# Kernel tuning notes

Hardware: AMD Instinct MI355X
Metric: run time of the kernel (lower is better)

The kernel has to match this reference:

```python
import jax, jax.numpy as jnp
import numpy as np
from jax import lax

OC, IC, K = 256, 256, 3
PAD, STRIDE = 1, 1
NNZ = 59000
N, H, W = 32, 56, 56


def setup_inputs() -> dict:
    key = jax.random.key(0)
    k1, k2, k3, k4 = jax.random.split(key, 4)
    x = jax.random.normal(k1, (N, IC, H, W), dtype=jnp.float32)
    W_val = jax.random.normal(k2, (NNZ,), dtype=jnp.float32)
    W_idx = jax.random.randint(k3, (NNZ,), 0, OC * IC * K * K, dtype=jnp.int64)
    bias = jax.random.normal(k4, (OC,), dtype=jnp.float32)
    return {"x": x, "W_val": W_val, "W_idx": W_idx, "bias": bias}


def reference(x, W_val, W_idx, bias):
    # Scatter COO values into the dense [OC, IC, K, K] weight (duplicates sum).
    dense_w = jnp.zeros((OC * IC * K * K,), dtype=W_val.dtype).at[W_idx].add(W_val)
    dense_w = dense_w.reshape(OC, IC, K, K)
    # conv2d, NCHW / OIHW layout, stride=STRIDE, symmetric padding=PAD
    out = lax.conv_general_dilated(
        x, dense_w,
        window_strides=(STRIDE, STRIDE),
        padding=[(PAD, PAD), (PAD, PAD)],
        dimension_numbers=("NCHW", "OIHW", "NCHW"),
    )
    out = out + bias[None, :, None, None]
    return out
```

## Files before the change

### kernel.cpp

```cpp
#include <hip/hip_runtime.h>

typedef unsigned short ushort;
typedef __attribute__((ext_vector_type(8))) short bf16x8;
typedef __attribute__((ext_vector_type(4))) float f32x4;
typedef __attribute__((ext_vector_type(4))) ushort us4;

#define NBATCH 32
#define ICN 256
#define OCN 256
#define HSZ 56
#define WSZ 56
#define HP 58
#define SPAT (HP*HP)
#define KTOT 2304
#define MTOT (NBATCH*HSZ*WSZ)
#define NT   (KTOT/64)
#define BM   224

#define XP_BYTES ((size_t)NBATCH*SPAT*ICN*2)
#define WD_BYTES ((size_t)OCN*KTOT*4)

__device__ __forceinline__ ushort f2bf(float f) {
  union { float f; unsigned u; } c; c.f = f;
  unsigned r = c.u + 0x7FFFu + ((c.u >> 16) & 1u);
  return (ushort)(r >> 16);
}

__global__ void k_transpose(const float* __restrict__ x, ushort* __restrict__ xp) {
  __shared__ ushort t2[WSZ*264];
  int h = blockIdx.x, n = blockIdx.y;
  ushort* dst = xp + ((size_t)n*SPAT + (size_t)h*HP)*ICN;
  if (h == 0 || h == HP-1) {
    for (int e = threadIdx.x; e < HP*ICN/4; e += 256) ((us4*)dst)[e] = (us4){0,0,0,0};
    return;
  }
  const float* src = x + ((size_t)n*ICN*HSZ*WSZ) + (size_t)(h-1)*WSZ;
  for (int e = threadIdx.x; e < ICN*WSZ; e += 256) {
    int ic = e / WSZ, w = e - ic*WSZ;
    t2[w*264 + ic] = f2bf(src[(size_t)ic*(HSZ*WSZ) + w]);
  }
  __syncthreads();
  for (int e4 = threadIdx.x; e4 < HP*ICN/4; e4 += 256) {
    int wp = e4 >> 6, ic4 = (e4 & 63) << 2;
    us4 v = (wp == 0 || wp == HP-1) ? (us4){0,0,0,0}
                                    : *(const us4*)&t2[(wp-1)*264 + ic4];
    ((us4*)dst)[e4] = v;
  }
}

__global__ void k_scatter(const int* __restrict__ idx, const float* __restrict__ val,
                          float* __restrict__ wd, int nnz) {
  int i = blockIdx.x*256 + threadIdx.x;
  if (i >= nnz) return;
  int id = idx[i];
  int oc = id / (ICN*9);
  int rem = id - oc*(ICN*9);
  int ic = rem / 9;
  int k9 = rem - ic*9;
  atomicAdd(wd + (size_t)oc*KTOT + k9*ICN + ic, val[i]);
}

__global__ void k_convert3(const float* __restrict__ wd, ushort* __restrict__ bm3) {
  int e = blockIdx.x*256 + threadIdx.x;
  int lam = e & 63;
  int f   = (e >> 6) & 3;
  int wc  = (e >> 8) & 3;
  int kh  = (e >> 10) & 1;
  int t   = e >> 11;
  int oc  = wc*64 + f*16 + (lam & 15);
  int k   = (t >> 2)*256 + (t & 3)*64 + kh*32 + (lam >> 4)*8;
  const float* src = wd + (size_t)oc*KTOT + k;
  float4 v0 = *(const float4*)(src);
  float4 v1 = *(const float4*)(src + 4);
  us4 lo, hi;
  lo[0]=f2bf(v0.x); lo[1]=f2bf(v0.y); lo[2]=f2bf(v0.z); lo[3]=f2bf(v0.w);
  hi[0]=f2bf(v1.x); hi[1]=f2bf(v1.y); hi[2]=f2bf(v1.z); hi[3]=f2bf(v1.w);
  ushort* dst = bm3 + (size_t)e*8;
  *(us4*)(dst) = lo; *(us4*)(dst+4) = hi;
}


#define GLD(gsrc, ldst) __builtin_amdgcn_global_load_lds( \
    (const __attribute__((address_space(1))) void*)(gsrc), \
    (__attribute__((address_space(3))) void*)(ldst), 16, 0, 0)
#define BAR()  asm volatile("s_barrier" ::: "memory")
#define VMW(N) do { asm volatile("s_waitcnt vmcnt(" #N ")" ::: "memory"); \
                    __builtin_amdgcn_sched_barrier(0); } while (0)
#define LGKM(N) do { asm volatile("s_waitcnt lgkmcnt(" #N ")" ::: "memory"); \
                     __builtin_amdgcn_sched_barrier(0); } while (0)

#define BUF_US  14848
#define BUF_B   29696

#define STAGE2X(T2, PAIR, BUFUS) do { \
    const int t4_ = (T2) >> 2; const int khh_ = t4_/3, khw_ = t4_ - khh_*3; \
    const int koff_ = (khh_*HP + khw_)*256 + (((T2) & 3) << 6); \
    ushort* b_ = Ab + (BUFUS); \
    GLD(xp + ((PAIR) ? sA2 : sA0) + koff_, b_ + ((PAIR) ? dO2 : dO0)); \
    GLD(xp + ((PAIR) ? sA3 : sA1) + koff_, b_ + ((PAIR) ? dO3 : dO1)); } while (0)

#define GLB(DST, VOFF) \
    asm volatile("global_load_dwordx4 %0, %4, %5 offset:0\n\t" \
                 "global_load_dwordx4 %1, %4, %5 offset:1024\n\t" \
                 "global_load_dwordx4 %2, %4, %5 offset:2048\n\t" \
                 "global_load_dwordx4 %3, %4, %5 offset:3072" \
                 : "=&v"(DST[0]), "=&v"(DST[1]), "=&v"(DST[2]), "=&v"(DST[3]) \
                 : "v"(VOFF), "s"(bm3) : "memory")

#define LOADA4(DST, KH, BFB) do { \
    unsigned a_ = ((KH) ? aL1v : aL0v) + (unsigned)(BFB); \
    asm volatile("ds_read_b128 %0, %4 offset:0\n\t" \
                 "ds_read_b128 %1, %4 offset:2048\n\t" \
                 "ds_read_b128 %2, %4 offset:4096\n\t" \
                 "ds_read_b128 %3, %4 offset:6144" \
                 : "=&v"(DST[0]), "=&v"(DST[1]), "=&v"(DST[2]), "=&v"(DST[3]) \
                 : "v"(a_)); } while (0)

#define LOADA3(DST, KH, BFB) do { \
    unsigned a_ = ((KH) ? aL1v : aL0v) + (unsigned)((BFB) + 8192); \
    asm volatile("ds_read_b128 %0, %3 offset:0\n\t" \
                 "ds_read_b128 %1, %3 offset:2048\n\t" \
                 "ds_read_b128 %2, %3 offset:4096" \
                 : "=&v"(DST[0]), "=&v"(DST[1]), "=&v"(DST[2]) \
                 : "v"(a_)); } while (0)

#define MFMA16(AV, BV) do { \
    __builtin_amdgcn_s_setprio(1); \
    _Pragma("unroll") \
    for (int f_ = 0; f_ < 4; ++f_) { \
      _Pragma("unroll") \
      for (int n_ = 0; n_ < 4; ++n_) \
        acc[f_][n_] = __builtin_amdgcn_mfma_f32_16x16x32_bf16( \
            AV[f_], BV[n_], acc[f_][n_], 0, 0, 0); \
    } \
    __builtin_amdgcn_s_setprio(0); } while (0)

#define MFMA12(AV, BV) do { \
    __builtin_amdgcn_s_setprio(1); \
    _Pragma("unroll") \
    for (int f_ = 0; f_ < 3; ++f_) { \
      _Pragma("unroll") \
      for (int n_ = 0; n_ < 4; ++n_) \
        acc[4+f_][n_] = __builtin_amdgcn_mfma_f32_16x16x32_bf16( \
            AV[f_], BV[n_], acc[4+f_][n_], 0, 0, 0); \
    } \
    __builtin_amdgcn_s_setprio(0); } while (0)

__global__ __launch_bounds__(512, 2) void k_gemm8(const ushort* __restrict__ xp,
                                                  const ushort* __restrict__ bm3,
                                                  const float* __restrict__ bias,
                                                  float* __restrict__ out) {
  __shared__ __align__(128) ushort Ab[3*BUF_US];

  const int tid = threadIdx.x;
  const int lam = tid & 63;
  const int wv  = tid >> 6;
  const int wr  = wv >> 2;
  const int wc  = wv & 3;
  const int la  = lam & 15;
  const int m0  = blockIdx.x * BM;

  const unsigned AbB = (unsigned)(uintptr_t)(__attribute__((address_space(3))) char*)Ab;

  const int q0 = (lam >> 4) ^ (la & 7);
  const unsigned aL0v = AbB + wr*14336 + la*128 + q0*16;
  const unsigned aL1v = AbB + wr*14336 + la*128 + (q0 ^ 4)*16;

  const unsigned wcB = wc*4096 + lam*16;

  int sA0, sA1, sA2, sA3;
  int dO0, dO1, dO2, dO3;
  if (wv < 7) {
    const int oA = (lam & 7) ^ (lam >> 3);
    int m, n, rem, oh, ow, r;
    r = (wv*4 + 0)*8 + (lam >> 3);
    m = m0 + r; n = m/3136; rem = m - n*3136; oh = rem/56; ow = rem - oh*56;
    sA0 = (n*SPAT + oh*HP + ow)*ICN + oA*8;  dO0 = (wv*4 + 0)*512;
    r = (wv*4 + 1)*8 + (lam >> 3);
    m = m0 + r; n = m/3136; rem = m - n*3136; oh = rem/56; ow = rem - oh*56;
    sA1 = (n*SPAT + oh*HP + ow)*ICN + oA*8;  dO1 = (wv*4 + 1)*512;
    r = (wv*4 + 2)*8 + (lam >> 3);
    m = m0 + r; n = m/3136; rem = m - n*3136; oh = rem/56; ow = rem - oh*56;
    sA2 = (n*SPAT + oh*HP + ow)*ICN + oA*8;  dO2 = (wv*4 + 2)*512;
    r = (wv*4 + 3)*8 + (lam >> 3);
    m = m0 + r; n = m/3136; rem = m - n*3136; oh = rem/56; ow = rem - oh*56;
    sA3 = (n*SPAT + oh*HP + ow)*ICN + oA*8;  dO3 = (wv*4 + 3)*512;
  } else {
    sA0 = sA1 = sA2 = sA3 = 0;
    dO0 = dO1 = dO2 = dO3 = 14336;
  }

  f32x4 acc[7][4];
#pragma unroll
  for (int a = 0; a < 7; ++a)
#pragma unroll
    for (int b = 0; b < 4; ++b) acc[a][b] = (f32x4){0.f, 0.f, 0.f, 0.f};

  bf16x8 avq0_[4], avq1_[3], avq2_[4], avq3_[3], bvA_[4], bvB_[4];

  STAGE2X(0, 0, 0);       STAGE2X(0, 1, 0);
  STAGE2X(1, 0, BUF_US);  STAGE2X(1, 1, BUF_US);
  GLB(bvA_, wcB);
  VMW(4);
  BAR();
  LOADA4(avq0_, 0, 0); LOADA3(avq1_, 0, 0);

  int bf0b = 0, bf1b = BUF_B, bf2b = 2*BUF_B;
  int bf2u = 2*BUF_US;
  for (int t = 0; t < NT-2; ++t) {
    const unsigned vb = (unsigned)t*32768 + wcB;
    LOADA4(avq2_, 1, bf0b);
    GLB(bvB_, vb + 16384);
    VMW(4);
    LGKM(7);
    MFMA16(avq0_, bvA_);
    LOADA3(avq3_, 1, bf0b);
    STAGE2X(t+2, 0, bf2u);
    LGKM(7);
    MFMA12(avq1_, bvA_);
    BAR();
    LOADA4(avq0_, 0, bf1b);
    STAGE2X(t+2, 1, bf2u);
    VMW(4);
    LGKM(7);
    MFMA16(avq2_, bvB_);
    LOADA3(avq1_, 0, bf1b);
    GLB(bvA_, vb + 32768);
    LGKM(7);
    MFMA12(avq3_, bvB_);
    BAR();
    int bt = bf0b; bf0b = bf1b; bf1b = bf2b; bf2b = bt;
    bf2u = bf2b / 2;
  }

  {
    const unsigned vb = (unsigned)(NT-2)*32768 + wcB;
    LOADA4(avq2_, 1, bf0b);
    GLB(bvB_, vb + 16384);
    VMW(4);
    LGKM(7);
    MFMA16(avq0_, bvA_);
    LOADA3(avq3_, 1, bf0b);
    LGKM(7);
    MFMA12(avq1_, bvA_);
    BAR();
    LOADA4(avq0_, 0, bf1b);
    VMW(0);
    LGKM(7);
    MFMA16(avq2_, bvB_);
    LOADA3(avq1_, 0, bf1b);
    GLB(bvA_, vb + 32768);
    LGKM(7);
    MFMA12(avq3_, bvB_);
    BAR();
    int bt = bf0b; bf0b = bf1b; bf1b = bf2b; bf2b = bt;
  }

  {
    const unsigned vb = (unsigned)(NT-1)*32768 + wcB;
    LOADA4(avq2_, 1, bf0b);
    GLB(bvB_, vb + 16384);
    VMW(4);
    LGKM(7);
    MFMA16(avq0_, bvA_);
    LOADA3(avq3_, 1, bf0b);
    LGKM(7);
    MFMA12(avq1_, bvA_);
    VMW(0);
    LGKM(3);
    MFMA16(avq2_, bvB_);
    LGKM(0);
    MFMA12(avq3_, bvB_);
  }

#pragma unroll
  for (int nn = 0; nn < 4; ++nn) {
    int oc = wc*64 + nn*16 + la;
    float bvs = bias[oc];
#pragma unroll
    for (int mf = 0; mf < 7; ++mf) {
      int m = m0 + wr*112 + mf*16 + ((lam >> 4) << 2);
      int n = m / 3136;
      int rem = m - n*3136;
      float4 o;
      o.x = acc[mf][nn][0] + bvs;
      o.y = acc[mf][nn][1] + bvs;
      o.z = acc[mf][nn][2] + bvs;
      o.w = acc[mf][nn][3] + bvs;
      *(float4*)(out + ((size_t)(n*OCN + oc))*3136 + rem) = o;
    }
  }
}

extern "C" void kernel_launch(void* const* d_in, const int* in_sizes, int n_in,
                              void* d_out, int out_size, void* d_ws, size_t ws_size,
                              hipStream_t stream) {
  const float* x    = (const float*)d_in[0];
  const float* wval = (const float*)d_in[1];
  const int*   widx = (const int*)d_in[2];
  const float* bias = (const float*)d_in[3];
  float* out = (float*)d_out;
  const int nnz = in_sizes[1];

  char* ws = (char*)d_ws;
  ushort* xp  = (ushort*)ws;
  float*  wd  = (float*)(ws + XP_BYTES);
  ushort* bm3 = (ushort*)(ws + XP_BYTES + WD_BYTES);

  hipMemsetAsync(wd, 0, WD_BYTES, stream);
  k_transpose<<<dim3(HP, NBATCH), 256, 0, stream>>>(x, xp);
  k_scatter<<<dim3((nnz + 255)/256), 256, 0, stream>>>(widx, wval, wd, nnz);
  k_convert3<<<dim3((NT*2*16*64)/256), 256, 0, stream>>>(wd, bm3);
  k_gemm8<<<dim3(MTOT/BM), 512, 0, stream>>>(xp, bm3, bias, out);
}
```

Baseline: 149.4 us.

## Restructure GEMM pipeline to double-buffered 128-wide K steps with per-wave half staging

Replaces the triple-buffered 64-wide K pipeline with a double-buffered loop that handles 128 K elements per iteration and uses half as many barriers. Each half of the waves stages one 64-wide K slice, seven rows per wave, so all 8 waves share the global-to-LDS loads. The global loads are interleaved with the MFMA groups under adjusted waitcnts. This cuts barrier and synchronisation overhead per K element, at the cost of a larger per-buffer LDS footprint and tighter wait-count bookkeeping.

Result: no change. 148.9 us (-0.4%).

```diff
diff --git a/kernel.cpp b/kernel.cpp
--- a/kernel.cpp
+++ b/kernel.cpp
@@ -14,7 +14,7 @@
 #define SPAT (HP*HP)
 #define KTOT 2304
 #define MTOT (NBATCH*HSZ*WSZ)
-#define NT   (KTOT/64)
+#define NT2  (KTOT/128)
 #define BM   224
 
 #define XP_BYTES ((size_t)NBATCH*SPAT*ICN*2)
@@ -89,15 +89,11 @@
 #define LGKM(N) do { asm volatile("s_waitcnt lgkmcnt(" #N ")" ::: "memory"); \
                      __builtin_amdgcn_sched_barrier(0); } while (0)
 
-#define BUF_US  14848
-#define BUF_B   29696
-
-#define STAGE2X(T2, PAIR, BUFUS) do { \
-    const int t4_ = (T2) >> 2; const int khh_ = t4_/3, khw_ = t4_ - khh_*3; \
-    const int koff_ = (khh_*HP + khw_)*256 + (((T2) & 3) << 6); \
-    ushort* b_ = Ab + (BUFUS); \
-    GLD(xp + ((PAIR) ? sA2 : sA0) + koff_, b_ + ((PAIR) ? dO2 : dO0)); \
-    GLD(xp + ((PAIR) ? sA3 : sA1) + koff_, b_ + ((PAIR) ? dO3 : dO1)); } while (0)
+#define BUF2_US 29184
+#define BUF2_B  58368
+
+#define STAGE1(SRC, DO, SU) \
+    GLD(xp + (SRC) + koffw, Ab + (SU) + (DO))
 
 #define GLB(DST, VOFF) \
     asm volatile("global_load_dwordx4 %0, %4, %5 offset:0\n\t" \
@@ -107,8 +103,8 @@
                  : "=&v"(DST[0]), "=&v"(DST[1]), "=&v"(DST[2]), "=&v"(DST[3]) \
                  : "v"(VOFF), "s"(bm3) : "memory")
 
-#define LOADA4(DST, KH, BFB) do { \
-    unsigned a_ = ((KH) ? aL1v : aL0v) + (unsigned)(BFB); \
+#define LOADA4(DST, BASE, OFF) do { \
+    unsigned a_ = (BASE) + (unsigned)(OFF); \
     asm volatile("ds_read_b128 %0, %4 offset:0\n\t" \
                  "ds_read_b128 %1, %4 offset:2048\n\t" \
                  "ds_read_b128 %2, %4 offset:4096\n\t" \
@@ -116,8 +112,8 @@
                  : "=&v"(DST[0]), "=&v"(DST[1]), "=&v"(DST[2]), "=&v"(DST[3]) \
                  : "v"(a_)); } while (0)
 
-#define LOADA3(DST, KH, BFB) do { \
-    unsigned a_ = ((KH) ? aL1v : aL0v) + (unsigned)((BFB) + 8192); \
+#define LOADA3(DST, BASE, OFF) do { \
+    unsigned a_ = (BASE) + (unsigned)((OFF) + 8192); \
     asm volatile("ds_read_b128 %0, %3 offset:0\n\t" \
                  "ds_read_b128 %1, %3 offset:2048\n\t" \
                  "ds_read_b128 %2, %3 offset:4096" \
@@ -150,7 +146,7 @@
                                                   const ushort* __restrict__ bm3,
                                                   const float* __restrict__ bias,
                                                   float* __restrict__ out) {
-  __shared__ __align__(128) ushort Ab[3*BUF_US];
+  __shared__ __align__(128) ushort Ab[2*BUF2_US];
 
   const int tid = threadIdx.x;
   const int lam = tid & 63;
@@ -158,6 +154,7 @@
   const int wr  = wv >> 2;
   const int wc  = wv & 3;
   const int la  = lam & 15;
+  const int hv  = wv >> 2;
   const int m0  = blockIdx.x * BM;
 
   const unsigned AbB = (unsigned)(uintptr_t)(__attribute__((address_space(3))) char*)Ab;
@@ -168,26 +165,21 @@
 
   const unsigned wcB = wc*4096 + lam*16;
 
-  int sA0, sA1, sA2, sA3;
-  int dO0, dO1, dO2, dO3;
-  if (wv < 7) {
-    const int oA = (lam & 7) ^ (lam >> 3);
-    int m, n, rem, oh, ow, r;
-    r = (wv*4 + 0)*8 + (lam >> 3);
-    m = m0 + r; n = m/3136; rem = m - n*3136; oh = rem/56; ow = rem - oh*56;
-    sA0 = (n*SPAT + oh*HP + ow)*ICN + oA*8;  dO0 = (wv*4 + 0)*512;
-    r = (wv*4 + 1)*8 + (lam >> 3);
-    m = m0 + r; n = m/3136; rem = m - n*3136; oh = rem/56; ow = rem - oh*56;
-    sA1 = (n*SPAT + oh*HP + ow)*ICN + oA*8;  dO1 = (wv*4 + 1)*512;
-    r = (wv*4 + 2)*8 + (lam >> 3);
-    m = m0 + r; n = m/3136; rem = m - n*3136; oh = rem/56; ow = rem - oh*56;
-    sA2 = (n*SPAT + oh*HP + ow)*ICN + oA*8;  dO2 = (wv*4 + 2)*512;
-    r = (wv*4 + 3)*8 + (lam >> 3);
-    m = m0 + r; n = m/3136; rem = m - n*3136; oh = rem/56; ow = rem - oh*56;
-    sA3 = (n*SPAT + oh*HP + ow)*ICN + oA*8;  dO3 = (wv*4 + 3)*512;
-  } else {
-    sA0 = sA1 = sA2 = sA3 = 0;
-    dO0 = dO1 = dO2 = dO3 = 14336;
+  int srcA0, srcA1, srcA2, srcA3, srcA4, srcA5, srcA6;
+  int dO0, dO1, dO2, dO3, dO4, dO5, dO6;
+  {
+    const int oA8 = ((lam & 7) ^ (lam >> 3)) * 8;
+    const int jb = (wv & 3)*7;
+    int m, n, rem, oh, ow;
+#define MKSRC(I, SV, DV) do { \
+    int row_ = (jb + (I))*8 + (lam >> 3); \
+    m = m0 + row_; n = m/3136; rem = m - n*3136; oh = rem/56; ow = rem - oh*56; \
+    SV = (n*SPAT + oh*HP + ow)*ICN + oA8; \
+    DV = hv*14336 + (jb + (I))*512; } while (0)
+    MKSRC(0, srcA0, dO0); MKSRC(1, srcA1, dO1); MKSRC(2, srcA2, dO2);
+    MKSRC(3, srcA3, dO3); MKSRC(4, srcA4, dO4); MKSRC(5, srcA5, dO5);
+    MKSRC(6, srcA6, dO6);
+#undef MKSRC
   }
 
   f32x4 acc[7][4];
@@ -198,79 +190,80 @@
 
   bf16x8 avq0_[4], avq1_[3], avq2_[4], avq3_[3], bvA_[4], bvB_[4];
 
-  STAGE2X(0, 0, 0);       STAGE2X(0, 1, 0);
-  STAGE2X(1, 0, BUF_US);  STAGE2X(1, 1, BUF_US);
+  {
+    const int t64 = hv;
+    const int t4_ = t64 >> 2; const int khh_ = t4_/3, khw_ = t4_ - khh_*3;
+    const int koffw = (khh_*HP + khw_)*256 + ((t64 & 3) << 6);
+    STAGE1(srcA0, dO0, 0); STAGE1(srcA1, dO1, 0); STAGE1(srcA2, dO2, 0);
+    STAGE1(srcA3, dO3, 0); STAGE1(srcA4, dO4, 0); STAGE1(srcA5, dO5, 0);
+    STAGE1(srcA6, dO6, 0);
+  }
   GLB(bvA_, wcB);
-  VMW(4);
+  GLB(bvB_, wcB + 16384);
+  VMW(8);
   BAR();
-  LOADA4(avq0_, 0, 0); LOADA3(avq1_, 0, 0);
-
-  int bf0b = 0, bf1b = BUF_B, bf2b = 2*BUF_B;
-  int bf2u = 2*BUF_US;
-  for (int t = 0; t < NT-2; ++t) {
-    const unsigned vb = (unsigned)t*32768 + wcB;
-    LOADA4(avq2_, 1, bf0b);
-    GLB(bvB_, vb + 16384);
-    VMW(4);
-    LGKM(7);
-    MFMA16(avq0_, bvA_);
-    LOADA3(avq3_, 1, bf0b);
-    STAGE2X(t+2, 0, bf2u);
-    LGKM(7);
-    MFMA12(avq1_, bvA_);
+
+  for (int t = 0; t < NT2-1; ++t) {
+    const unsigned rb = (unsigned)((t & 1) ? BUF2_B : 0);
+    const int su = ((t & 1) ^ 1) * BUF2_US;
+    const unsigned vb = (unsigned)t*65536 + wcB;
+    int koffw;
+    {
+      const int t64 = 2*(t+1) + hv;
+      const int t4_ = t64 >> 2; const int khh_ = t4_/3, khw_ = t4_ - khh_*3;
+      koffw = (khh_*HP + khw_)*256 + ((t64 & 3) << 6);
+    }
+    LOADA4(avq0_, aL0v, rb); LOADA3(avq1_, aL0v, rb);
+    STAGE1(srcA0, dO0, su);
+    VMW(5);  LGKM(3);  MFMA16(avq0_, bvA_);
+    LOADA4(avq2_, aL1v, rb);
+    STAGE1(srcA1, dO1, su);
+    LGKM(4);  MFMA12(avq1_, bvA_);
+    LOADA3(avq3_, aL1v, rb);
+    STAGE1(srcA2, dO2, su);
+    GLB(bvA_, vb + 32768);
+    VMW(7);  LGKM(3);  MFMA16(avq2_, bvB_);
+    LOADA4(avq0_, aL0v, rb + 28672);
+    STAGE1(srcA3, dO3, su);
+    LGKM(4);  MFMA12(avq3_, bvB_);
+    LOADA3(avq1_, aL0v, rb + 28672);
+    STAGE1(srcA4, dO4, su);
+    GLB(bvB_, vb + 49152);
+    VMW(6);  LGKM(3);  MFMA16(avq0_, bvA_);
+    LOADA4(avq2_, aL1v, rb + 28672);
+    STAGE1(srcA5, dO5, su);
+    LGKM(4);  MFMA12(avq1_, bvA_);
+    LOADA3(avq3_, aL1v, rb + 28672);
+    STAGE1(srcA6, dO6, su);
+    GLB(bvA_, vb + 65536);
+    VMW(6);  LGKM(3);  MFMA16(avq2_, bvB_);
+    LGKM(0);  MFMA12(avq3_, bvB_);
+    GLB(bvB_, vb + 81920);
+    VMW(8);
     BAR();
-    LOADA4(avq0_, 0, bf1b);
-    STAGE2X(t+2, 1, bf2u);
-    VMW(4);
-    LGKM(7);
-    MFMA16(avq2_, bvB_);
-    LOADA3(avq1_, 0, bf1b);
+  }
+
+  {
+    const int t = NT2-1;
+    const unsigned rb = (unsigned)((t & 1) ? BUF2_B : 0);
+    const unsigned vb = (unsigned)t*65536 + wcB;
+    LOADA4(avq0_, aL0v, rb); LOADA3(avq1_, aL0v, rb);
+    VMW(4);  LGKM(3);  MFMA16(avq0_, bvA_);
+    LOADA4(avq2_, aL1v, rb);
+    LGKM(4);  MFMA12(avq1_, bvA_);
+    LOADA3(avq3_, aL1v, rb);
     GLB(bvA_, vb + 32768);
-    LGKM(7);
-    MFMA12(avq3_, bvB_);
-    BAR();
-    int bt = bf0b; bf0b = bf1b; bf1b = bf2b; bf2b = bt;
-    bf2u = bf2b / 2;
-  }
-
-  {
-    const unsigned vb = (unsigned)(NT-2)*32768 + wcB;
-    LOADA4(avq2_, 1, bf0b);
-    GLB(bvB_, vb + 16384);
-    VMW(4);
-    LGKM(7);
-    MFMA16(avq0_, bvA_);
-    LOADA3(avq3_, 1, bf0b);
-    LGKM(7);
-    MFMA12(avq1_, bvA_);
-    BAR();
-    LOADA4(avq0_, 0, bf1b);
-    VMW(0);
-    LGKM(7);
-    MFMA16(avq2_, bvB_);
-    LOADA3(avq1_, 0, bf1b);
-    GLB(bvA_, vb + 32768);
-    LGKM(7);
-    MFMA12(avq3_, bvB_);
-    BAR();
-    int bt = bf0b; bf0b = bf1b; bf1b = bf2b; bf2b = bt;
-  }
-
-  {
-    const unsigned vb = (unsigned)(NT-1)*32768 + wcB;
-    LOADA4(avq2_, 1, bf0b);
-    GLB(bvB_, vb + 16384);
-    VMW(4);
-    LGKM(7);
-    MFMA16(avq0_, bvA_);
-    LOADA3(avq3_, 1, bf0b);
-    LGKM(7);
-    MFMA12(avq1_, bvA_);
-    VMW(0);
-    LGKM(3);
-    MFMA16(avq2_, bvB_);
-    LGKM(0);
-    MFMA12(avq3_, bvB_);
+    VMW(4);  LGKM(3);  MFMA16(avq2_, bvB_);
+    LOADA4(avq0_, aL0v, rb + 28672);
+    LGKM(4);  MFMA12(avq3_, bvB_);
+    LOADA3(avq1_, aL0v, rb + 28672);
+    GLB(bvB_, vb + 49152);
+    VMW(4);  LGKM(3);  MFMA16(avq0_, bvA_);
+    LOADA4(avq2_, aL1v, rb + 28672);
+    LGKM(4);  MFMA12(avq1_, bvA_);
+    LOADA3(avq3_, aL1v, rb + 28672);
+    VMW(0);  LGKM(3);  MFMA16(avq2_, bvB_);
+    LGKM(0);  MFMA12(avq3_, bvB_);
   }
 
 #pragma unroll
@@ -310,6 +303,6 @@
   hipMemsetAsync(wd, 0, WD_BYTES, stream);
   k_transpose<<<dim3(HP, NBATCH), 256, 0, stream>>>(x, xp);
   k_scatter<<<dim3((nnz + 255)/256), 256, 0, stream>>>(widx, wval, wd, nnz);
-  k_convert3<<<dim3((NT*2*16*64)/256), 256, 0, stream>>>(wd, bm3);
+  k_convert3<<<dim3((KTOT/64*2*16*64)/256), 256, 0, stream>>>(wd, bm3);
   k_gemm8<<<dim3(MTOT/BM), 512, 0, stream>>>(xp, bm3, bias, out);
 }
```

## Split main loop by wave row with finer-grained MFMA/LDS interleave

Applied to the files above, without the earlier changes.

Waves in the second row (wr!=0) now run a different main-loop schedule. Their MFMA groups are split into smaller chunks, and the LDS fragment loads and global staging are interleaved between those chunks under explicit scheduling barriers. Waves in the first row keep the original schedule. The aim is to desynchronize the two wave rows so that LDS reads and MFMA issue overlap better across waves, which reduces LDS bank contention and MFMA idle time. The cost is code duplication and more delicate waitcnt accounting (lgkmcnt values) that could stall or be subtly wrong.

Result: no change. 150.7 us (+0.9%).

```diff
diff --git a/kernel.cpp b/kernel.cpp
--- a/kernel.cpp
+++ b/kernel.cpp
@@ -88,6 +88,7 @@
                     __builtin_amdgcn_sched_barrier(0); } while (0)
 #define LGKM(N) do { asm volatile("s_waitcnt lgkmcnt(" #N ")" ::: "memory"); \
                      __builtin_amdgcn_sched_barrier(0); } while (0)
+#define SB() __builtin_amdgcn_sched_barrier(0)
 
 #define BUF_US  14848
 #define BUF_B   29696
@@ -146,6 +147,47 @@
     } \
     __builtin_amdgcn_s_setprio(0); } while (0)
 
+#define MFMA8_01(AV, BV) do { \
+    __builtin_amdgcn_s_setprio(1); \
+    _Pragma("unroll") \
+    for (int f_ = 0; f_ < 2; ++f_) { \
+      _Pragma("unroll") \
+      for (int n_ = 0; n_ < 4; ++n_) \
+        acc[f_][n_] = __builtin_amdgcn_mfma_f32_16x16x32_bf16( \
+            AV[f_], BV[n_], acc[f_][n_], 0, 0, 0); \
+    } \
+    __builtin_amdgcn_s_setprio(0); } while (0)
+
+#define MFMA8_23(AV, BV) do { \
+    __builtin_amdgcn_s_setprio(1); \
+    _Pragma("unroll") \
+    for (int f_ = 2; f_ < 4; ++f_) { \
+      _Pragma("unroll") \
+      for (int n_ = 0; n_ < 4; ++n_) \
+        acc[f_][n_] = __builtin_amdgcn_mfma_f32_16x16x32_bf16( \
+            AV[f_], BV[n_], acc[f_][n_], 0, 0, 0); \
+    } \
+    __builtin_amdgcn_s_setprio(0); } while (0)
+
+#define MFMA4_0(AV, BV) do { \
+    __builtin_amdgcn_s_setprio(1); \
+    _Pragma("unroll") \
+    for (int n_ = 0; n_ < 4; ++n_) \
+      acc[4][n_] = __builtin_amdgcn_mfma_f32_16x16x32_bf16( \
+          AV[0], BV[n_], acc[4][n_], 0, 0, 0); \
+    __builtin_amdgcn_s_setprio(0); } while (0)
+
+#define MFMA8_12(AV, BV) do { \
+    __builtin_amdgcn_s_setprio(1); \
+    _Pragma("unroll") \
+    for (int f_ = 1; f_ < 3; ++f_) { \
+      _Pragma("unroll") \
+      for (int n_ = 0; n_ < 4; ++n_) \
+        acc[4+f_][n_] = __builtin_amdgcn_mfma_f32_16x16x32_bf16( \
+            AV[f_], BV[n_], acc[4+f_][n_], 0, 0, 0); \
+    } \
+    __builtin_amdgcn_s_setprio(0); } while (0)
+
 __global__ __launch_bounds__(512, 2) void k_gemm8(const ushort* __restrict__ xp,
                                                   const ushort* __restrict__ bm3,
                                                   const float* __restrict__ bias,
@@ -165,7 +207,6 @@
   const int q0 = (lam >> 4) ^ (la & 7);
   const unsigned aL0v = AbB + wr*14336 + la*128 + q0*16;
   const unsigned aL1v = AbB + wr*14336 + la*128 + (q0 ^ 4)*16;
-
   const unsigned wcB = wc*4096 + lam*16;
 
   int sA0, sA1, sA2, sA3;
@@ -207,30 +248,69 @@
 
   int bf0b = 0, bf1b = BUF_B, bf2b = 2*BUF_B;
   int bf2u = 2*BUF_US;
-  for (int t = 0; t < NT-2; ++t) {
-    const unsigned vb = (unsigned)t*32768 + wcB;
-    LOADA4(avq2_, 1, bf0b);
-    GLB(bvB_, vb + 16384);
-    VMW(4);
-    LGKM(7);
-    MFMA16(avq0_, bvA_);
-    LOADA3(avq3_, 1, bf0b);
-    STAGE2X(t+2, 0, bf2u);
-    LGKM(7);
-    MFMA12(avq1_, bvA_);
-    BAR();
-    LOADA4(avq0_, 0, bf1b);
-    STAGE2X(t+2, 1, bf2u);
-    VMW(4);
-    LGKM(7);
-    MFMA16(avq2_, bvB_);
-    LOADA3(avq1_, 0, bf1b);
-    GLB(bvA_, vb + 32768);
-    LGKM(7);
-    MFMA12(avq3_, bvB_);
-    BAR();
-    int bt = bf0b; bf0b = bf1b; bf1b = bf2b; bf2b = bt;
-    bf2u = bf2b / 2;
+  if (wr == 0) {
+    for (int t = 0; t < NT-2; ++t) {
+      const unsigned vb = (unsigned)t*32768 + wcB;
+      LOADA4(avq2_, 1, bf0b);
+      GLB(bvB_, vb + 16384);
+      VMW(4);
+      LGKM(7);
+      MFMA16(avq0_, bvA_);
+      LOADA3(avq3_, 1, bf0b);
+      STAGE2X(t+2, 0, bf2u);
+      LGKM(7);
+      MFMA12(avq1_, bvA_);
+      BAR();
+      LOADA4(avq0_, 0, bf1b);
+      STAGE2X(t+2, 1, bf2u);
+      VMW(4);
+      LGKM(7);
+      MFMA16(avq2_, bvB_);
+      LOADA3(avq1_, 0, bf1b);
+      GLB(bvA_, vb + 32768);
+      LGKM(7);
+      MFMA12(avq3_, bvB_);
+      BAR();
+      int bt = bf0b; bf0b = bf1b; bf1b = bf2b; bf2b = bt;
+      bf2u = bf2b / 2;
+    }
+  } else {
+    for (int t = 0; t < NT-2; ++t) {
+      const unsigned vb = (unsigned)t*32768 + wcB;
+      GLB(bvB_, vb + 16384);
+      VMW(4);
+      LGKM(0);
+      MFMA8_01(avq0_, bvA_);
+      SB();
+      LOADA4(avq2_, 1, bf0b);
+      SB();
+      MFMA8_23(avq0_, bvA_);
+      STAGE2X(t+2, 0, bf2u);
+      MFMA4_0(avq1_, bvA_);
+      SB();
+      LOADA3(avq3_, 1, bf0b);
+      SB();
+      MFMA8_12(avq1_, bvA_);
+      BAR();
+      STAGE2X(t+2, 1, bf2u);
+      VMW(4);
+      LGKM(3);
+      MFMA8_01(avq2_, bvB_);
+      SB();
+      LOADA4(avq0_, 0, bf1b);
+      SB();
+      MFMA8_23(avq2_, bvB_);
+      GLB(bvA_, vb + 32768);
+      LGKM(4);
+      MFMA4_0(avq3_, bvB_);
+      SB();
+      LOADA3(avq1_, 0, bf1b);
+      SB();
+      MFMA8_12(avq3_, bvB_);
+      BAR();
+      int bt = bf0b; bf0b = bf1b; bf1b = bf2b; bf2b = bt;
+      bf2u = bf2b / 2;
+    }
   }
 
   {
```
